# Kernel optimization log

Hardware: AMD Instinct MI355X
Metric: run time of the kernel (lower is better)

## Reference

```python
import jax, jax.numpy as jnp
import numpy as np

NUM_HEADS = 16
ROPE_THETA = 10000.0


def setup_inputs() -> dict:
    key = jax.random.key(0)
    k1, k2, k3 = jax.random.split(key, 3)
    B, S, D = 2, 2048, 1024
    std_qkv = float(np.sqrt(2.0 / (D + 3 * D)))
    std_out = float(np.sqrt(2.0 / (D + D)))
    return {
        "x": jax.random.normal(k1, (B, S, D), dtype=jnp.float32),
        "qkv_w": jax.random.normal(k2, (3 * D, D), dtype=jnp.float32) * std_qkv,
        "out_w": jax.random.normal(k3, (D, D), dtype=jnp.float32) * std_out,
        "token_positions": jnp.arange(S, dtype=jnp.int32),
    }


def _apply_rope(x, token_positions, theta=ROPE_THETA):
    # x: [B, H, S, d_k], token_positions: [S]
    d_k = x.shape[-1]
    inv_freqs = 1.0 / (theta ** (jnp.arange(0, d_k, 2, dtype=jnp.float32) / d_k))  # [d_k/2]
    angles = token_positions.astype(jnp.float32)[:, None] * inv_freqs[None, :]     # [S, d_k/2]
    cos, sin = jnp.cos(angles), jnp.sin(angles)
    x_even, x_odd = x[..., 0::2], x[..., 1::2]
    r_even = x_even * cos - x_odd * sin
    r_odd = x_even * sin + x_odd * cos
    # interleave back: [..., d_k/2, 2] -> [..., d_k]
    return jnp.stack([r_even, r_odd], axis=-1).reshape(x.shape)


def reference(x, qkv_w, out_w, token_positions):
    B, S, D = x.shape
    H = NUM_HEADS
    d_k = D // H

    qkv = jnp.einsum("bsd,ed->bse", x, qkv_w)                  # [B, S, 3*D]
    qkv = qkv.reshape(B, S, 3, H, d_k)
    q, k, v = (jnp.transpose(qkv[:, :, i], (0, 2, 1, 3)) for i in range(3))  # each [B, H, S, d_k]

    q = _apply_rope(q, token_positions)
    k = _apply_rope(k, token_positions)

    scale = 1.0 / jnp.sqrt(jnp.asarray(d_k, dtype=x.dtype))
    scores = jnp.einsum("bhqd,bhkd->bhqk", q, k) * scale       # [B, H, S, S]
    causal = jnp.tril(jnp.ones((S, S), dtype=bool))
    scores = jnp.where(causal, scores, jnp.asarray(-jnp.inf, dtype=scores.dtype))
    attn = jax.nn.softmax(scores, axis=-1)
    out = jnp.einsum("bhqk,bhkd->bhqd", attn, v)               # [B, H, S, d_k]
    out = jnp.transpose(out, (0, 2, 1, 3)).reshape(B, S, D)    # [B, S, D]
    return jnp.einsum("bsd,ed->bse", out, out_w)               # [B, S, D]
```

## Files before the change

kernel.cpp:

```cpp
#include <hip/hip_runtime.h>

typedef __bf16 bf16x8 __attribute__((ext_vector_type(8)));
typedef __bf16 bf16x2 __attribute__((ext_vector_type(2)));
typedef float f32x4 __attribute__((ext_vector_type(4)));
typedef unsigned short u16;
typedef u16 u16x8 __attribute__((ext_vector_type(8)));
typedef u16 u16x2 __attribute__((ext_vector_type(2)));

__device__ __forceinline__ u16 f2bf(float f) {
    union { float f; unsigned u; } x; x.f = f;
    unsigned r = x.u + 0x7fffu + ((x.u >> 16) & 1u);
    return (u16)(r >> 16);
}
__device__ __forceinline__ bf16x8 as_bf16x8(u16x8 v) {
    return __builtin_bit_cast(bf16x8, v);
}
__device__ __forceinline__ void glds16(const void* g, void* l) {
    __builtin_amdgcn_global_load_lds(
        (const __attribute__((address_space(1))) void*)g,
        (__attribute__((address_space(3))) void*)l, 16, 0, 0);
}
__device__ __forceinline__ int swz(int r) { return (((r & 7) ^ ((r >> 3) & 7)) << 3); }
__device__ __forceinline__ int pswz(int r) { return (((r >> 2) & 3) << 3); }

__global__ __launch_bounds__(256) void f32bf16(const float* __restrict__ in,
                                               u16* __restrict__ out, int n8) {
    int i = blockIdx.x * 256 + threadIdx.x;
    if (i >= n8) return;
    const float4* p = (const float4*)(in + (size_t)i * 8);
    float4 a = p[0], b = p[1];
    u16x8 o;
    o[0] = f2bf(a.x); o[1] = f2bf(a.y); o[2] = f2bf(a.z); o[3] = f2bf(a.w);
    o[4] = f2bf(b.x); o[5] = f2bf(b.y); o[6] = f2bf(b.z); o[7] = f2bf(b.w);
    *(u16x8*)(out + (size_t)i * 8) = o;
}

__global__ __launch_bounds__(256) void gemm128(const u16* __restrict__ A,
                                               const u16* __restrict__ B,
                                               float* __restrict__ C,
                                               int N, int K, int nbx) {
    __shared__ u16 As[2][4096];
    __shared__ u16 Bs[2][4096];
    const int tid = threadIdx.x, lane = tid & 63, wave = tid >> 6;
    const int cpx = gridDim.x >> 3;
    const int nid = (blockIdx.x & 7) * cpx + (blockIdx.x >> 3);
    const int m0 = (nid / nbx) << 7, n0 = (nid % nbx) << 7;
    const int wr = (wave >> 1) << 6, wc = (wave & 1) << 6;
    const int fr = lane & 15, fo = (lane >> 4) << 3;
    const int srow = tid >> 2, scol = (tid & 3) << 3;
    const u16* Ag = A + (size_t)(m0 + srow) * K + scol;
    const u16* Bg = B + (size_t)(n0 + srow) * K + scol;
    u16* AsW = &As[0][0] + (wave << 9);
    u16* BsW = &Bs[0][0] + (wave << 9);
    f32x4 acc[4][4] = {};
    const int nsteps = K >> 5;
    glds16(Ag, AsW);
    glds16(Ag + (size_t)64 * K, AsW + 2048);
    glds16(Bg, BsW);
    glds16(Bg + (size_t)64 * K, BsW + 2048);
    int cur = 0;
    for (int s = 0; s < nsteps; ++s) {
        __syncthreads();
        if (s + 1 < nsteps) {
            const u16* Ap = Ag + (s + 1) * 32;
            const u16* Bp = Bg + (s + 1) * 32;
            const int nb = (cur ^ 1) << 12;
            glds16(Ap, AsW + nb);
            glds16(Ap + (size_t)64 * K, AsW + nb + 2048);
            glds16(Bp, BsW + nb);
            glds16(Bp + (size_t)64 * K, BsW + nb + 2048);
        }
        const u16* Ab = &As[cur][0];
        const u16* Bb = &Bs[cur][0];
        bf16x8 af[4], bfr[4];
        #pragma unroll
        for (int i = 0; i < 4; ++i)
            af[i] = *(const bf16x8*)(Ab + (wr + i * 16 + fr) * 32 + fo);
        #pragma unroll
        for (int i = 0; i < 4; ++i)
            bfr[i] = *(const bf16x8*)(Bb + (wc + i * 16 + fr) * 32 + fo);
        #pragma unroll
        for (int i = 0; i < 4; ++i)
            #pragma unroll
            for (int j = 0; j < 4; ++j)
                acc[i][j] = __builtin_amdgcn_mfma_f32_16x16x32_bf16(af[i], bfr[j], acc[i][j], 0, 0, 0);
        cur ^= 1;
    }
    const int cr = (lane >> 4) << 2, cc = lane & 15;
    #pragma unroll
    for (int i = 0; i < 4; ++i)
        for (int j = 0; j < 4; ++j)
            for (int r = 0; r < 4; ++r)
                C[(size_t)(m0 + wr + i * 16 + cr + r) * N + (n0 + wc + j * 16 + cc)] = acc[i][j][r];
}

__global__ __launch_bounds__(256) void rope_split(const float* __restrict__ qkv,
                                                  const int* __restrict__ pos,
                                                  u16* __restrict__ Qb,
                                                  u16* __restrict__ Kb) {
    int tid = blockIdx.x * 256 + threadIdx.x;
    int t = tid & 31;
    int h = (tid >> 5) & 15;
    int s = (tid >> 9) & 2047;
    int b = tid >> 20;
    const float* row = qkv + (size_t)((b << 11) + s) * 3072;
    float fp  = (float)pos[s];
    float inv = powf(10000.0f, -(float)(2 * t) * (1.0f / 64.0f));
    float angle = fp * inv;
    float sn, cs;
    sincosf(angle, &sn, &cs);
    int off = h * 64 + 2 * t;
    float2 q2 = *(const float2*)(row + off);
    float2 k2 = *(const float2*)(row + 1024 + off);
    size_t oidx = (((size_t)(b * 16 + h) * 2048) + s) * 64 + 2 * t;
    const float qs = 0.18033688011112042f;
    u16x2 qo, ko;
    qo[0] = f2bf((q2.x * cs - q2.y * sn) * qs);
    qo[1] = f2bf((q2.x * sn + q2.y * cs) * qs);
    ko[0] = f2bf(k2.x * cs - k2.y * sn);
    ko[1] = f2bf(k2.x * sn + k2.y * cs);
    *(u16x2*)&Qb[oidx] = qo;
    *(u16x2*)&Kb[oidx] = ko;
}

__global__ __launch_bounds__(256) void vtrans(const float* __restrict__ qkv,
                                              u16* __restrict__ Vt) {
    __shared__ u16 lds[64][72];
    const int t = threadIdx.x;
    const int st = blockIdx.x, h = blockIdx.y, b = blockIdx.z;
    const int s0 = st << 6;
    {
        const int r = t >> 2, c0 = (t & 3) << 4;
        const float* src = qkv + (size_t)((b << 11) + s0 + r) * 3072 + 2048 + h * 64 + c0;
        const float4* p = (const float4*)src;
        #pragma unroll
        for (int q = 0; q < 4; ++q) {
            float4 v = p[q];
            lds[r][c0 + q * 4 + 0] = f2bf(v.x);
            lds[r][c0 + q * 4 + 1] = f2bf(v.y);
            lds[r][c0 + q * 4 + 2] = f2bf(v.z);
            lds[r][c0 + q * 4 + 3] = f2bf(v.w);
        }
    }
    __syncthreads();
    const size_t obase = ((size_t)((b << 4) + h) << 17) + (st << 6);
    #pragma unroll
    for (int w = 0; w < 2; ++w) {
        const int q = t + (w << 8);
        const int d = q >> 3, c = q & 7;
        u16x8 o;
        #pragma unroll
        for (int i = 0; i < 8; ++i) {
            const int p  = (c << 3) + i;
            const int hh = p >> 5, qq = p & 31;
            const int k  = (hh << 5) + ((qq & 1) << 4) + (qq >> 1);
            o[i] = lds[k][d];
        }
        *(u16x8*)(Vt + obase + ((size_t)d << 11) + (c << 3)) = o;
    }
}

__global__ __launch_bounds__(512, 4) void attn_causal(const u16* __restrict__ Q,
                                                      const u16* __restrict__ K,
                                                      const u16* __restrict__ Vt,
                                                      u16* __restrict__ O) {
    __shared__ u16 smem[20480];
    __shared__ float cmb[5120];
    const int tid = threadIdx.x, lane = tid & 63, wave = tid >> 6;
    const int nid = ((blockIdx.x & 7) << 6) + (blockIdx.x >> 3);
    const int pr = nid & 15, h = (nid >> 4) & 15, b = nid >> 8;
    const int S = 2048;
    const size_t base = (size_t)((b << 4) + h) << 17;
    const int fr = lane & 15, fo = (lane >> 4) << 3, cr = (lane >> 4) << 2;
    const int schk = lane & 7, srow8 = lane >> 3;
    const int qsub = wave >> 1, half = wave & 1;
    u16* const Psw = smem + 16384 + (wave << 9);
    float* const slot = cmb + qsub * 1280 + lane * 20;
    u16x8 ones_u;
    #pragma unroll
    for (int i = 0; i < 8; ++i) ones_u[i] = 0x3F80;
    const bf16x8 ones = as_bf16x8(ones_u);

    auto stage = [&](int t, int bi) {
        const int r  = (wave << 3) + srow8;
        const int ck = (schk ^ srow8 ^ wave) << 3;
        glds16(K  + base + ((size_t)((t << 6) + r) << 6) + ck,
               &smem[(bi << 12) + (wave << 9)]);
        glds16(Vt + base + ((size_t)r << 11) + (t << 6) + ck,
               &smem[8192 + (bi << 12) + (wave << 9)]);
    };

    for (int phase = 0; phase < 2; ++phase) {
        const int qt = phase ? (31 - pr) : pr;
        const int nkt = qt + 1;
        const int qw = (qt << 6) + (qsub << 4);
        bf16x8 aq0, aq1;
        {
            const u16* qrow = Q + base + (size_t)(qw + fr) * 64;
            aq0 = as_bf16x8(*(const u16x8*)(qrow + fo));
            aq1 = as_bf16x8(*(const u16x8*)(qrow + 32 + fo));
        }
        f32x4 oacc[4] = {};
        f32x4 lacc = {};
        stage(0, 0);
        for (int t = 0; t < nkt; ++t) {
            __syncthreads();
            if (t + 1 < nkt) stage(t + 1, (t + 1) & 1);
            const u16* Kb = smem + ((t & 1) << 12);
            const u16* Vb = smem + 8192 + ((t & 1) << 12);
            const bool diag = (t == nkt - 1);
            f32x4 sacc[2];
            #pragma unroll
            for (int ch = 0; ch < 2; ++ch) {
                const int r = ((half << 1) + ch) * 16 + fr;
                const int sw = swz(r);
                bf16x8 bk0 = *(const bf16x8*)&Kb[r * 64 + (fo ^ sw)];
                bf16x8 bk1 = *(const bf16x8*)&Kb[r * 64 + ((32 + fo) ^ sw)];
                f32x4 sc = {};
                sc = __builtin_amdgcn_mfma_f32_16x16x32_bf16(aq0, bk0, sc, 0, 0, 0);
                sc = __builtin_amdgcn_mfma_f32_16x16x32_bf16(aq1, bk1, sc, 0, 0, 0);
                sacc[ch] = sc;
            }
            #pragma unroll
            for (int j = 0; j < 4; ++j) {
                const int prow = cr + j;
                bf16x2 pk;
                #pragma unroll
                for (int ch = 0; ch < 2; ++ch) {
                    float e = exp2f(sacc[ch][j]);
                    if (diag) {
                        const int cglob = (half << 1) + ch;
                        const bool keep = (cglob < qsub) | ((cglob == qsub) & (fr <= prow));
                        e = keep ? e : 0.f;
                    }
                    pk[ch] = (__bf16)e;
                }
                *(bf16x2*)&Psw[prow * 32 + ((fr << 1) ^ pswz(prow))] = pk;
            }
            bf16x8 pa = *(const bf16x8*)&Psw[fr * 32 + (fo ^ pswz(fr))];
            lacc = __builtin_amdgcn_mfma_f32_16x16x32_bf16(pa, ones, lacc, 0, 0, 0);
            #pragma unroll
            for (int tt = 0; tt < 4; ++tt) {
                const int d = tt * 16 + fr;
                bf16x8 bv = *(const bf16x8*)&Vb[d * 64 + (((half << 5) + fo) ^ swz(d))];
                oacc[tt] = __builtin_amdgcn_mfma_f32_16x16x32_bf16(pa, bv, oacc[tt], 0, 0, 0);
            }
        }
        __syncthreads();
        if (half) {
            #pragma unroll
            for (int tt = 0; tt < 4; ++tt) *(f32x4*)(slot + tt * 4) = oacc[tt];
            *(f32x4*)(slot + 16) = lacc;
        }
        __syncthreads();
        if (!half) {
            #pragma unroll
            for (int tt = 0; tt < 4; ++tt) oacc[tt] += *(const f32x4*)(slot + tt * 4);
            lacc += *(const f32x4*)(slot + 16);
            f32x4 inv;
            #pragma unroll
            for (int j = 0; j < 4; ++j) inv[j] = 1.f / lacc[j];
            #pragma unroll
            for (int tt = 0; tt < 4; ++tt)
                for (int j = 0; j < 4; ++j)
                    O[(size_t)(b * S + qw + cr + j) * 1024 + h * 64 + tt * 16 + fr] =
                        f2bf(oacc[tt][j] * inv[j]);
        }
        __syncthreads();
    }
}

extern "C" void kernel_launch(void* const* d_in, const int* in_sizes, int n_in,
                              void* d_out, int out_size, void* d_ws, size_t ws_size,
                              hipStream_t stream) {
    const float* x     = (const float*)d_in[0];
    const float* qkv_w = (const float*)d_in[1];
    const float* out_w = (const float*)d_in[2];
    const int*   pos   = (const int*)d_in[3];
    float* out = (float*)d_out;

    char* ws = (char*)d_ws;
    float* qkv  = (float*)ws;
    u16*   Qb   = (u16*)(ws + 50331648);
    u16*   Kb   = (u16*)(ws + 58720256);
    u16*   Vtg  = (u16*)(ws + 67108864);
    u16*   x16  = (u16*)(ws + 75497472);
    u16*   att16= (u16*)(ws + 75497472);
    u16*   w16  = (u16*)(ws + 83886080);
    u16*   ow16 = (u16*)(ws + 90177536);

    f32bf16<<<2048, 256, 0, stream>>>(x, x16, 524288);
    f32bf16<<<1536, 256, 0, stream>>>(qkv_w, w16, 393216);
    f32bf16<<<512, 256, 0, stream>>>(out_w, ow16, 131072);
    gemm128<<<768, 256, 0, stream>>>(x16, w16, qkv, 3072, 1024, 24);
    rope_split<<<8192, 256, 0, stream>>>(qkv, pos, Qb, Kb);
    vtrans<<<dim3(32, 16, 2), 256, 0, stream>>>(qkv, Vtg);
    attn_causal<<<512, 512, 0, stream>>>(Qb, Kb, Vtg, att16);
    gemm128<<<256, 256, 0, stream>>>(att16, ow16, out, 1024, 1024, 8);
}
```

Baseline: 132.8 us.

## Emit bf16 QKV from GEMM, keep P in registers via transposed MFMA

The QKV projection GEMM now writes bf16 instead of fp32, which halves the intermediate traffic that rope_split and vtrans read. The attention kernel swaps the MFMA operands so the score fragment already has the A-operand layout for the PV product. This removes the LDS round trip for P and shrinks shared memory. RoPE trig switches to exp2 plus the hardware sin/cos on a range-reduced angle, and V's key permutation is adjusted to match the new P layout. Rounding qkv to bf16 before RoPE adds a small amount of precision loss.

```diff
diff --git a/kernel.cpp b/kernel.cpp
--- a/kernel.cpp
+++ b/kernel.cpp
@@ -1,7 +1,6 @@
 #include <hip/hip_runtime.h>
 
 typedef __bf16 bf16x8 __attribute__((ext_vector_type(8)));
-typedef __bf16 bf16x2 __attribute__((ext_vector_type(2)));
 typedef float f32x4 __attribute__((ext_vector_type(4)));
 typedef unsigned short u16;
 typedef u16 u16x8 __attribute__((ext_vector_type(8)));
@@ -12,6 +11,10 @@
     unsigned r = x.u + 0x7fffu + ((x.u >> 16) & 1u);
     return (u16)(r >> 16);
 }
+__device__ __forceinline__ float bf2f(u16 v) {
+    union { unsigned u; float f; } x; x.u = ((unsigned)v) << 16;
+    return x.f;
+}
 __device__ __forceinline__ bf16x8 as_bf16x8(u16x8 v) {
     return __builtin_bit_cast(bf16x8, v);
 }
@@ -21,7 +24,6 @@
         (__attribute__((address_space(3))) void*)l, 16, 0, 0);
 }
 __device__ __forceinline__ int swz(int r) { return (((r & 7) ^ ((r >> 3) & 7)) << 3); }
-__device__ __forceinline__ int pswz(int r) { return (((r >> 2) & 3) << 3); }
 
 __global__ __launch_bounds__(256) void f32bf16(const float* __restrict__ in,
                                                u16* __restrict__ out, int n8) {
@@ -35,9 +37,10 @@
     *(u16x8*)(out + (size_t)i * 8) = o;
 }
 
+template<bool BF16OUT>
 __global__ __launch_bounds__(256) void gemm128(const u16* __restrict__ A,
                                                const u16* __restrict__ B,
-                                               float* __restrict__ C,
+                                               void* __restrict__ Cv,
                                                int N, int K, int nbx) {
     __shared__ u16 As[2][4096];
     __shared__ u16 Bs[2][4096];
@@ -87,14 +90,26 @@
         cur ^= 1;
     }
     const int cr = (lane >> 4) << 2, cc = lane & 15;
-    #pragma unroll
-    for (int i = 0; i < 4; ++i)
-        for (int j = 0; j < 4; ++j)
-            for (int r = 0; r < 4; ++r)
-                C[(size_t)(m0 + wr + i * 16 + cr + r) * N + (n0 + wc + j * 16 + cc)] = acc[i][j][r];
-}
-
-__global__ __launch_bounds__(256) void rope_split(const float* __restrict__ qkv,
+    if constexpr (BF16OUT) {
+        u16* C = (u16*)Cv;
+        #pragma unroll
+        for (int i = 0; i < 4; ++i)
+            for (int j = 0; j < 4; ++j)
+                for (int r = 0; r < 4; ++r)
+                    C[(size_t)(m0 + wr + i * 16 + cr + r) * N + (n0 + wc + j * 16 + cc)] =
+                        f2bf(acc[i][j][r]);
+    } else {
+        float* C = (float*)Cv;
+        #pragma unroll
+        for (int i = 0; i < 4; ++i)
+            for (int j = 0; j < 4; ++j)
+                for (int r = 0; r < 4; ++r)
+                    C[(size_t)(m0 + wr + i * 16 + cr + r) * N + (n0 + wc + j * 16 + cc)] =
+                        acc[i][j][r];
+    }
+}
+
+__global__ __launch_bounds__(256) void rope_split(const u16* __restrict__ qkv,
                                                   const int* __restrict__ pos,
                                                   u16* __restrict__ Qb,
                                                   u16* __restrict__ Kb) {
@@ -103,27 +118,30 @@
     int h = (tid >> 5) & 15;
     int s = (tid >> 9) & 2047;
     int b = tid >> 20;
-    const float* row = qkv + (size_t)((b << 11) + s) * 3072;
+    const u16* row = qkv + (size_t)((b << 11) + s) * 3072;
     float fp  = (float)pos[s];
-    float inv = powf(10000.0f, -(float)(2 * t) * (1.0f / 64.0f));
-    float angle = fp * inv;
-    float sn, cs;
-    sincosf(angle, &sn, &cs);
+    float inv = exp2f((float)t * -0.4152410118609203f);
+    float rev = fp * inv * 0.15915494309189535f;
+    rev = rev - floorf(rev);
+    float sn = __builtin_amdgcn_sinf(rev);
+    float cs = __builtin_amdgcn_cosf(rev);
     int off = h * 64 + 2 * t;
-    float2 q2 = *(const float2*)(row + off);
-    float2 k2 = *(const float2*)(row + 1024 + off);
+    u16x2 q2 = *(const u16x2*)(row + off);
+    u16x2 k2 = *(const u16x2*)(row + 1024 + off);
+    float qx = bf2f(q2[0]), qy = bf2f(q2[1]);
+    float kx = bf2f(k2[0]), ky = bf2f(k2[1]);
     size_t oidx = (((size_t)(b * 16 + h) * 2048) + s) * 64 + 2 * t;
     const float qs = 0.18033688011112042f;
     u16x2 qo, ko;
-    qo[0] = f2bf((q2.x * cs - q2.y * sn) * qs);
-    qo[1] = f2bf((q2.x * sn + q2.y * cs) * qs);
-    ko[0] = f2bf(k2.x * cs - k2.y * sn);
-    ko[1] = f2bf(k2.x * sn + k2.y * cs);
+    qo[0] = f2bf((qx * cs - qy * sn) * qs);
+    qo[1] = f2bf((qx * sn + qy * cs) * qs);
+    ko[0] = f2bf(kx * cs - ky * sn);
+    ko[1] = f2bf(ky * cs + kx * sn);
     *(u16x2*)&Qb[oidx] = qo;
     *(u16x2*)&Kb[oidx] = ko;
 }
 
-__global__ __launch_bounds__(256) void vtrans(const float* __restrict__ qkv,
+__global__ __launch_bounds__(256) void vtrans(const u16* __restrict__ qkv,
                                               u16* __restrict__ Vt) {
     __shared__ u16 lds[64][72];
     const int t = threadIdx.x;
@@ -131,16 +149,9 @@
     const int s0 = st << 6;
     {
         const int r = t >> 2, c0 = (t & 3) << 4;
-        const float* src = qkv + (size_t)((b << 11) + s0 + r) * 3072 + 2048 + h * 64 + c0;
-        const float4* p = (const float4*)src;
-        #pragma unroll
-        for (int q = 0; q < 4; ++q) {
-            float4 v = p[q];
-            lds[r][c0 + q * 4 + 0] = f2bf(v.x);
-            lds[r][c0 + q * 4 + 1] = f2bf(v.y);
-            lds[r][c0 + q * 4 + 2] = f2bf(v.z);
-            lds[r][c0 + q * 4 + 3] = f2bf(v.w);
-        }
+        const u16* src = qkv + (size_t)((b << 11) + s0 + r) * 3072 + 2048 + h * 64 + c0;
+        *(u16x8*)&lds[r][c0]     = *(const u16x8*)src;
+        *(u16x8*)&lds[r][c0 + 8] = *(const u16x8*)(src + 8);
     }
     __syncthreads();
     const size_t obase = ((size_t)((b << 4) + h) << 17) + (st << 6);
@@ -151,9 +162,9 @@
         u16x8 o;
         #pragma unroll
         for (int i = 0; i < 8; ++i) {
-            const int p  = (c << 3) + i;
-            const int hh = p >> 5, qq = p & 31;
-            const int k  = (hh << 5) + ((qq & 1) << 4) + (qq >> 1);
+            const int p = (c << 3) + i;
+            const int k = ((p >> 5) << 5) + (((p >> 3) & 3) << 2) + (p & 3)
+                        + (((p >> 2) & 1) << 4);
             o[i] = lds[k][d];
         }
         *(u16x8*)(Vt + obase + ((size_t)d << 11) + (c << 3)) = o;
@@ -164,7 +175,7 @@
                                                       const u16* __restrict__ K,
                                                       const u16* __restrict__ Vt,
                                                       u16* __restrict__ O) {
-    __shared__ u16 smem[20480];
+    __shared__ u16 smem[16384];
     __shared__ float cmb[5120];
     const int tid = threadIdx.x, lane = tid & 63, wave = tid >> 6;
     const int nid = ((blockIdx.x & 7) << 6) + (blockIdx.x >> 3);
@@ -174,7 +185,6 @@
     const int fr = lane & 15, fo = (lane >> 4) << 3, cr = (lane >> 4) << 2;
     const int schk = lane & 7, srow8 = lane >> 3;
     const int qsub = wave >> 1, half = wave & 1;
-    u16* const Psw = smem + 16384 + (wave << 9);
     float* const slot = cmb + qsub * 1280 + lane * 20;
     u16x8 ones_u;
     #pragma unroll
@@ -202,6 +212,7 @@
         }
         f32x4 oacc[4] = {};
         f32x4 lacc = {};
+        const int qloc = (qsub << 4) + fr;
         stage(0, 0);
         for (int t = 0; t < nkt; ++t) {
             __syncthreads();
@@ -217,27 +228,24 @@
                 bf16x8 bk0 = *(const bf16x8*)&Kb[r * 64 + (fo ^ sw)];
                 bf16x8 bk1 = *(const bf16x8*)&Kb[r * 64 + ((32 + fo) ^ sw)];
                 f32x4 sc = {};
-                sc = __builtin_amdgcn_mfma_f32_16x16x32_bf16(aq0, bk0, sc, 0, 0, 0);
-                sc = __builtin_amdgcn_mfma_f32_16x16x32_bf16(aq1, bk1, sc, 0, 0, 0);
+                sc = __builtin_amdgcn_mfma_f32_16x16x32_bf16(bk0, aq0, sc, 0, 0, 0);
+                sc = __builtin_amdgcn_mfma_f32_16x16x32_bf16(bk1, aq1, sc, 0, 0, 0);
                 sacc[ch] = sc;
             }
-            #pragma unroll
-            for (int j = 0; j < 4; ++j) {
-                const int prow = cr + j;
-                bf16x2 pk;
+            bf16x8 pa;
+            #pragma unroll
+            for (int ch = 0; ch < 2; ++ch) {
+                const int cglob = (half << 1) + ch;
                 #pragma unroll
-                for (int ch = 0; ch < 2; ++ch) {
-                    float e = exp2f(sacc[ch][j]);
+                for (int r = 0; r < 4; ++r) {
+                    float e = exp2f(sacc[ch][r]);
                     if (diag) {
-                        const int cglob = (half << 1) + ch;
-                        const bool keep = (cglob < qsub) | ((cglob == qsub) & (fr <= prow));
-                        e = keep ? e : 0.f;
+                        const int kloc = (cglob << 4) + cr + r;
+                        e = (kloc <= qloc) ? e : 0.f;
                     }
-                    pk[ch] = (__bf16)e;
+                    pa[ch * 4 + r] = (__bf16)e;
                 }
-                *(bf16x2*)&Psw[prow * 32 + ((fr << 1) ^ pswz(prow))] = pk;
             }
-            bf16x8 pa = *(const bf16x8*)&Psw[fr * 32 + (fo ^ pswz(fr))];
             lacc = __builtin_amdgcn_mfma_f32_16x16x32_bf16(pa, ones, lacc, 0, 0, 0);
             #pragma unroll
             for (int tt = 0; tt < 4; ++tt) {
@@ -280,21 +288,21 @@
     float* out = (float*)d_out;
 
     char* ws = (char*)d_ws;
-    float* qkv  = (float*)ws;
-    u16*   Qb   = (u16*)(ws + 50331648);
-    u16*   Kb   = (u16*)(ws + 58720256);
-    u16*   Vtg  = (u16*)(ws + 67108864);
-    u16*   x16  = (u16*)(ws + 75497472);
-    u16*   att16= (u16*)(ws + 75497472);
-    u16*   w16  = (u16*)(ws + 83886080);
-    u16*   ow16 = (u16*)(ws + 90177536);
+    u16* qkv16 = (u16*)ws;
+    u16* Qb    = (u16*)(ws + 25165824);
+    u16* Kb    = (u16*)(ws + 33554432);
+    u16* Vtg   = (u16*)(ws + 41943040);
+    u16* x16   = (u16*)(ws + 50331648);
+    u16* att16 = (u16*)(ws + 50331648);
+    u16* w16   = (u16*)(ws + 58720256);
+    u16* ow16  = (u16*)(ws + 65011712);
 
     f32bf16<<<2048, 256, 0, stream>>>(x, x16, 524288);
     f32bf16<<<1536, 256, 0, stream>>>(qkv_w, w16, 393216);
     f32bf16<<<512, 256, 0, stream>>>(out_w, ow16, 131072);
-    gemm128<<<768, 256, 0, stream>>>(x16, w16, qkv, 3072, 1024, 24);
-    rope_split<<<8192, 256, 0, stream>>>(qkv, pos, Qb, Kb);
-    vtrans<<<dim3(32, 16, 2), 256, 0, stream>>>(qkv, Vtg);
+    gemm128<true><<<768, 256, 0, stream>>>(x16, w16, (void*)qkv16, 3072, 1024, 24);
+    rope_split<<<8192, 256, 0, stream>>>(qkv16, pos, Qb, Kb);
+    vtrans<<<dim3(32, 16, 2), 256, 0, stream>>>(qkv16, Vtg);
     attn_causal<<<512, 512, 0, stream>>>(Qb, Kb, Vtg, att16);
-    gemm128<<<256, 256, 0, stream>>>(att16, ow16, out, 1024, 1024, 8);
-}
+    gemm128<false><<<256, 256, 0, stream>>>(att16, ow16, (void*)out, 1024, 1024, 8);
+}
```

Result: faster. 121.8 us (-8.3%).
